# Kernel tuning notes

Measured on AMD Instinct MI355X. Metric: run time of the kernel, lower is better.

Reference implementation:

```python
import jax, jax.numpy as jnp
import numpy as np

N_NODES = 50000
N_EDGES = 800000
D_FEAT = 64


def setup_inputs() -> dict:
    key = jax.random.key(0)
    k1, k2 = jax.random.split(key)
    x = jax.random.normal(k1, (N_NODES, D_FEAT), dtype=jnp.float32)
    edge_index = jax.random.randint(k2, (2, N_EDGES), 0, N_NODES, dtype=jnp.int64)
    return {"x": x, "edge_index": edge_index}


def reference(x, edge_index):
    # flow = 'source_to_target': j (source) = edge_index[0], i (target) = edge_index[1]
    src, dst = edge_index[0], edge_index[1]
    # __lift__: gather source-node features per edge -> message(x_j) = x_j
    msg = x[src]                                   # [E, D]
    # aggregate: scatter-add into target nodes (aggr='add', dim_size = N)
    out = jax.ops.segment_sum(msg, dst, num_segments=x.shape[0])  # [N, D]
    # update: identity
    return out
```

## Files before the change

### kernel.cpp

```cpp
#include <hip/hip_runtime.h>
#include <hip/hip_bf16.h>


#define N_NODES_C 50000
#define D_FEAT_C 64
#define NXCD 8
#define NPR ((N_NODES_C + NXCD - 1) / NXCD)
#define SLOTS 64
#define OVF_CAP 65536

static_assert(N_NODES_C < 65536, "src/dst must fit 16 bits");

typedef int v4i __attribute__((ext_vector_type(4)));
typedef float v4f __attribute__((ext_vector_type(4)));

__device__ __forceinline__ void fill_one(int d, int s, int* __restrict__ cnt,
                                         unsigned short* __restrict__ slots,
                                         unsigned int* __restrict__ ovf,
                                         int* __restrict__ ovf_cnt) {
    int p = atomicAdd(&cnt[d], 1);
    if (p < SLOTS) {
        slots[(size_t)d * SLOTS + p] = (unsigned short)s;
    } else {
        int i = atomicAdd(ovf_cnt, 1);
        if (i < OVF_CAP) ovf[i] = (unsigned)s | ((unsigned)d << 16);
    }
}

__global__ void __launch_bounds__(256) k_fill(const int* __restrict__ src,
                                              const int* __restrict__ dst,
                                              int* __restrict__ cnt,
                                              unsigned short* __restrict__ slots,
                                              unsigned int* __restrict__ ovf,
                                              int* __restrict__ ovf_cnt, int E) {
    const int range = blockIdx.x & (NXCD - 1);
    const int sub   = blockIdx.x >> 3;
    const int nsub  = gridDim.x >> 3;
    const int lo = range * NPR;
    const int hi = lo + NPR;

    const int n4 = E >> 2;
    const v4i* s4 = (const v4i*)src;
    const v4i* d4 = (const v4i*)dst;
    const int start = sub * blockDim.x + threadIdx.x;
    const int stride = nsub * blockDim.x;

    for (int j = start; j < n4; j += stride) {
        v4i d = d4[j];
        bool m0 = (d.x >= lo) & (d.x < hi);
        bool m1 = (d.y >= lo) & (d.y < hi);
        bool m2 = (d.z >= lo) & (d.z < hi);
        bool m3 = (d.w >= lo) & (d.w < hi);
        if (m0 | m1 | m2 | m3) {
            v4i s = s4[j];
            if (m0) fill_one(d.x, s.x, cnt, slots, ovf, ovf_cnt);
            if (m1) fill_one(d.y, s.y, cnt, slots, ovf, ovf_cnt);
            if (m2) fill_one(d.z, s.z, cnt, slots, ovf, ovf_cnt);
            if (m3) fill_one(d.w, s.w, cnt, slots, ovf, ovf_cnt);
        }
    }
    for (int j = (n4 << 2) + start; j < E; j += stride) {
        int d = dst[j];
        if (d >= lo && d < hi) fill_one(d, src[j], cnt, slots, ovf, ovf_cnt);
    }
}

__global__ void __launch_bounds__(256) k_gather3(const float* __restrict__ x,
                                                 const unsigned short* __restrict__ slots,
                                                 const int* __restrict__ cnt,
                                                 const unsigned int* __restrict__ ovf,
                                                 const int* __restrict__ ovf_cnt,
                                                 float* __restrict__ out) {
    int node = blockIdx.x * 4 + (threadIdx.x >> 6);
    if (node >= N_NODES_C) return;
    const int t = threadIdx.x & 63;
    const int g = t >> 4;
    const int q = t & 15;

    const int c = cnt[node];
    const int m = c < SLOTS ? c : SLOTS;
    const unsigned short* sl = slots + (size_t)node * SLOTS;

    v4f acc = {0.f, 0.f, 0.f, 0.f};
    #pragma unroll 2
    for (int k = 0; k < m; k += 4) {
        unsigned long long pk = *(const unsigned long long*)(sl + k);
        int e = k + g;
        if (e < m) {
            int s = (int)((pk >> (16 * g)) & 0xFFFFull);
            v4f v = *(const v4f*)(x + (size_t)s * D_FEAT_C + q * 4);
            acc += v;
        }
    }

    if (c > SLOTS) {
        int L = *ovf_cnt; if (L > OVF_CAP) L = OVF_CAP;
        for (int i = 0; i < L; ++i) {
            unsigned p = ovf[i];
            if ((int)(p >> 16) == node && g == 0) {
                v4f v = *(const v4f*)(x + (size_t)(p & 0xFFFFu) * D_FEAT_C + q * 4);
                acc += v;
            }
        }
    }

    #pragma unroll
    for (int off = 16; off <= 32; off <<= 1) {
        acc.x += __shfl_xor(acc.x, off, 64);
        acc.y += __shfl_xor(acc.y, off, 64);
        acc.z += __shfl_xor(acc.z, off, 64);
        acc.w += __shfl_xor(acc.w, off, 64);
    }
    if (g == 0) *(v4f*)(out + (size_t)node * D_FEAT_C + q * 4) = acc;
}

extern "C" void kernel_launch(void* const* d_in, const int* in_sizes, int n_in,
                              void* d_out, int out_size, void* d_ws, size_t ws_size,
                              hipStream_t stream) {
    const float* x = (const float*)d_in[0];
    const int* edge_index = (const int*)d_in[1];
    float* out = (float*)d_out;

    const int E = in_sizes[1] / 2;
    const int* src = edge_index;
    const int* dst = edge_index + E;

    int* cnt = (int*)d_ws;
    int* ovf_cnt = cnt + N_NODES_C;
    unsigned int* ovf = (unsigned int*)(cnt + N_NODES_C + 4);
    unsigned short* slots = (unsigned short*)(ovf + OVF_CAP);

    (void)hipMemsetAsync(cnt, 0, (size_t)(N_NODES_C + 1) * sizeof(int), stream);

    k_fill<<<1024, 256, 0, stream>>>(src, dst, cnt, slots, ovf, ovf_cnt, E);

    const int gridN = (N_NODES_C + 3) / 4;
    k_gather3<<<gridN, 256, 0, stream>>>(x, slots, cnt, ovf, ovf_cnt, out);
}
```

Before: 139.8 us.

## Fuse memset, fill and gather into one cooperative kernel with grid syncs

Replaces the memset plus two kernel launches with a single cooperative kernel. It zeroes the counters, builds the per-node slot lists, then gathers and sums features, with grid-wide syncs between the phases. The aim is to cut launch and inter-kernel gaps. In exchange, the gather phase now runs as a grid-stride loop over a fixed 2048-block grid instead of one block per four nodes, and grid.sync adds its own barrier overhead. The cooperative launch also requires all 2048 blocks to be resident at once.

After: 458.7 us. +228.1%, slower.

```diff
diff --git a/kernel.cpp b/kernel.cpp
--- a/kernel.cpp
+++ b/kernel.cpp
@@ -1,5 +1,8 @@
 #include <hip/hip_runtime.h>
 #include <hip/hip_bf16.h>
+#include <hip/hip_cooperative_groups.h>
+
+namespace cg = cooperative_groups;
 
 
 #define N_NODES_C 50000
@@ -8,6 +11,7 @@
 #define NPR ((N_NODES_C + NXCD - 1) / NXCD)
 #define SLOTS 64
 #define OVF_CAP 65536
+#define GRID_B 2048
 
 static_assert(N_NODES_C < 65536, "src/dst must fit 16 bits");
 
@@ -27,91 +31,98 @@
     }
 }
 
-__global__ void __launch_bounds__(256) k_fill(const int* __restrict__ src,
-                                              const int* __restrict__ dst,
-                                              int* __restrict__ cnt,
-                                              unsigned short* __restrict__ slots,
-                                              unsigned int* __restrict__ ovf,
-                                              int* __restrict__ ovf_cnt, int E) {
-    const int range = blockIdx.x & (NXCD - 1);
-    const int sub   = blockIdx.x >> 3;
-    const int nsub  = gridDim.x >> 3;
-    const int lo = range * NPR;
-    const int hi = lo + NPR;
+__global__ void __launch_bounds__(256, 8) k_all(const float* __restrict__ x,
+                                                const int* __restrict__ src,
+                                                const int* __restrict__ dst,
+                                                int* __restrict__ cnt,
+                                                unsigned short* __restrict__ slots,
+                                                unsigned int* __restrict__ ovf,
+                                                int* __restrict__ ovf_cnt,
+                                                float* __restrict__ out, int E) {
+    cg::grid_group grid = cg::this_grid();
+    const int t = threadIdx.x;
+    const int gtid = blockIdx.x * 256 + t;
+    const int nthr = gridDim.x * 256;
 
-    const int n4 = E >> 2;
-    const v4i* s4 = (const v4i*)src;
-    const v4i* d4 = (const v4i*)dst;
-    const int start = sub * blockDim.x + threadIdx.x;
-    const int stride = nsub * blockDim.x;
+    for (int i = gtid; i <= N_NODES_C; i += nthr) cnt[i] = 0;
+    grid.sync();
 
-    for (int j = start; j < n4; j += stride) {
-        v4i d = d4[j];
-        bool m0 = (d.x >= lo) & (d.x < hi);
-        bool m1 = (d.y >= lo) & (d.y < hi);
-        bool m2 = (d.z >= lo) & (d.z < hi);
-        bool m3 = (d.w >= lo) & (d.w < hi);
-        if (m0 | m1 | m2 | m3) {
-            v4i s = s4[j];
-            if (m0) fill_one(d.x, s.x, cnt, slots, ovf, ovf_cnt);
-            if (m1) fill_one(d.y, s.y, cnt, slots, ovf, ovf_cnt);
-            if (m2) fill_one(d.z, s.z, cnt, slots, ovf, ovf_cnt);
-            if (m3) fill_one(d.w, s.w, cnt, slots, ovf, ovf_cnt);
+    {
+        const int range = blockIdx.x & (NXCD - 1);
+        const int sub   = blockIdx.x >> 3;
+        const int nsub  = gridDim.x >> 3;
+        const int lo = range * NPR;
+        const int hi = lo + NPR;
+
+        const int n4 = E >> 2;
+        const v4i* s4 = (const v4i*)src;
+        const v4i* d4 = (const v4i*)dst;
+        const int start = sub * 256 + t;
+        const int stride = nsub * 256;
+
+        for (int j = start; j < n4; j += stride) {
+            v4i d = d4[j];
+            bool m0 = (d.x >= lo) & (d.x < hi);
+            bool m1 = (d.y >= lo) & (d.y < hi);
+            bool m2 = (d.z >= lo) & (d.z < hi);
+            bool m3 = (d.w >= lo) & (d.w < hi);
+            if (m0 | m1 | m2 | m3) {
+                v4i s = s4[j];
+                if (m0) fill_one(d.x, s.x, cnt, slots, ovf, ovf_cnt);
+                if (m1) fill_one(d.y, s.y, cnt, slots, ovf, ovf_cnt);
+                if (m2) fill_one(d.z, s.z, cnt, slots, ovf, ovf_cnt);
+                if (m3) fill_one(d.w, s.w, cnt, slots, ovf, ovf_cnt);
+            }
+        }
+        for (int j = (n4 << 2) + start; j < E; j += stride) {
+            int d = dst[j];
+            if (d >= lo && d < hi) fill_one(d, src[j], cnt, slots, ovf, ovf_cnt);
         }
     }
-    for (int j = (n4 << 2) + start; j < E; j += stride) {
-        int d = dst[j];
-        if (d >= lo && d < hi) fill_one(d, src[j], cnt, slots, ovf, ovf_cnt);
-    }
-}
+    grid.sync();
 
-__global__ void __launch_bounds__(256) k_gather3(const float* __restrict__ x,
-                                                 const unsigned short* __restrict__ slots,
-                                                 const int* __restrict__ cnt,
-                                                 const unsigned int* __restrict__ ovf,
-                                                 const int* __restrict__ ovf_cnt,
-                                                 float* __restrict__ out) {
-    int node = blockIdx.x * 4 + (threadIdx.x >> 6);
-    if (node >= N_NODES_C) return;
-    const int t = threadIdx.x & 63;
-    const int g = t >> 4;
-    const int q = t & 15;
+    {
+        const int wave = t >> 6;
+        const int lane = t & 63;
+        const int g = lane >> 4;
+        const int q = lane & 15;
+        const int node_stride = gridDim.x * 4;
 
-    const int c = cnt[node];
-    const int m = c < SLOTS ? c : SLOTS;
-    const unsigned short* sl = slots + (size_t)node * SLOTS;
+        for (int node = blockIdx.x * 4 + wave; node < N_NODES_C; node += node_stride) {
+            const int c = cnt[node];
+            const int m = c < SLOTS ? c : SLOTS;
+            const unsigned short* sl = slots + (size_t)node * SLOTS;
 
-    v4f acc = {0.f, 0.f, 0.f, 0.f};
-    #pragma unroll 2
-    for (int k = 0; k < m; k += 4) {
-        unsigned long long pk = *(const unsigned long long*)(sl + k);
-        int e = k + g;
-        if (e < m) {
-            int s = (int)((pk >> (16 * g)) & 0xFFFFull);
-            v4f v = *(const v4f*)(x + (size_t)s * D_FEAT_C + q * 4);
-            acc += v;
+            v4f acc = {0.f, 0.f, 0.f, 0.f};
+            #pragma unroll 2
+            for (int k = 0; k < m; k += 4) {
+                unsigned long long pk = *(const unsigned long long*)(sl + k);
+                int e = k + g;
+                if (e < m) {
+                    int s = (int)((pk >> (16 * g)) & 0xFFFFull);
+                    acc += *(const v4f*)(x + (size_t)s * D_FEAT_C + q * 4);
+                }
+            }
+
+            if (c > SLOTS) {
+                int L = *ovf_cnt; if (L > OVF_CAP) L = OVF_CAP;
+                for (int i = 0; i < L; ++i) {
+                    unsigned p = ovf[i];
+                    if ((int)(p >> 16) == node && g == 0)
+                        acc += *(const v4f*)(x + (size_t)(p & 0xFFFFu) * D_FEAT_C + q * 4);
+                }
+            }
+
+            #pragma unroll
+            for (int off = 16; off <= 32; off <<= 1) {
+                acc.x += __shfl_xor(acc.x, off, 64);
+                acc.y += __shfl_xor(acc.y, off, 64);
+                acc.z += __shfl_xor(acc.z, off, 64);
+                acc.w += __shfl_xor(acc.w, off, 64);
+            }
+            if (g == 0) *(v4f*)(out + (size_t)node * D_FEAT_C + q * 4) = acc;
         }
     }
-
-    if (c > SLOTS) {
-        int L = *ovf_cnt; if (L > OVF_CAP) L = OVF_CAP;
-        for (int i = 0; i < L; ++i) {
-            unsigned p = ovf[i];
-            if ((int)(p >> 16) == node && g == 0) {
-                v4f v = *(const v4f*)(x + (size_t)(p & 0xFFFFu) * D_FEAT_C + q * 4);
-                acc += v;
-            }
-        }
-    }
-
-    #pragma unroll
-    for (int off = 16; off <= 32; off <<= 1) {
-        acc.x += __shfl_xor(acc.x, off, 64);
-        acc.y += __shfl_xor(acc.y, off, 64);
-        acc.z += __shfl_xor(acc.z, off, 64);
-        acc.w += __shfl_xor(acc.w, off, 64);
-    }
-    if (g == 0) *(v4f*)(out + (size_t)node * D_FEAT_C + q * 4) = acc;
 }
 
 extern "C" void kernel_launch(void* const* d_in, const int* in_sizes, int n_in,
@@ -121,19 +132,18 @@
     const int* edge_index = (const int*)d_in[1];
     float* out = (float*)d_out;
 
-    const int E = in_sizes[1] / 2;
+    int E = in_sizes[1] / 2;
     const int* src = edge_index;
     const int* dst = edge_index + E;
 
     int* cnt = (int*)d_ws;
+    unsigned int* ovf = (unsigned int*)(cnt + N_NODES_C + 4);
     int* ovf_cnt = cnt + N_NODES_C;
-    unsigned int* ovf = (unsigned int*)(cnt + N_NODES_C + 4);
     unsigned short* slots = (unsigned short*)(ovf + OVF_CAP);
 
-    (void)hipMemsetAsync(cnt, 0, (size_t)(N_NODES_C + 1) * sizeof(int), stream);
-
-    k_fill<<<1024, 256, 0, stream>>>(src, dst, cnt, slots, ovf, ovf_cnt, E);
-
-    const int gridN = (N_NODES_C + 3) / 4;
-    k_gather3<<<gridN, 256, 0, stream>>>(x, slots, cnt, ovf, ovf_cnt, out);
+    void* args[] = { (void*)&x, (void*)&src, (void*)&dst, (void*)&cnt,
+                     (void*)&slots, (void*)&ovf, (void*)&ovf_cnt,
+                     (void*)&out, (void*)&E };
+    (void)hipLaunchCooperativeKernel((void*)k_all, dim3(GRID_B), dim3(256),
+                                     args, 0, stream);
 }
```
